# Kernel tuning notes

Measured on AMD Instinct MI355X. Metric: run time of the kernel, lower is better.

## Reference

```python
import jax, jax.numpy as jnp
import numpy as np

N, E = 50000, 250000
SD, VM = 128, 64          # scalar channels, vector multiplicity (irreps: 128x0e + 64x1e)
EA, SH = 64, 4            # edge_attr dim, spherical-harmonics dim (1x0e + 1x1e)
H, FC = 16, 256
HD = FC // H              # head dim = 16
EPS = 1e-5


def _split(x):
    return x[:, :SD], x[:, SD:].reshape(-1, VM, 3)


def _ln(s, V):
    # equivariant layer norm: standardize scalars; RMS-normalize vector norms
    s = (s - s.mean(-1, keepdims=True)) * jax.lax.rsqrt(s.var(-1, keepdims=True) + EPS)
    vn = jax.lax.rsqrt(jnp.mean(jnp.sum(V * V, -1), -1, keepdims=True) + EPS)
    return s, V * vn[..., None]


def setup_inputs() -> dict:
    key = jax.random.key(0)
    ks = iter(jax.random.split(key, 48))
    rn = lambda shp, sc=1.0: jax.random.normal(next(ks), shp, dtype=jnp.float32) * sc
    w = lambda i, o: rn((i, o), 1.0 / np.sqrt(i))
    z = lambda d: jnp.zeros((d,), jnp.float32)
    return dict(
        node_features=rn((N, SD + 3 * VM)),
        edge_attr=rn((E, EA)),
        edge_sh=rn((E, SH)),
        Wq=w(SD, FC), bq=z(FC),
        Wk=w(SD, FC), bk=z(FC),
        We=w(EA, FC), be=z(FC),
        Wv_s=w(SD, SD), bv_s=z(SD), Wv_v=w(VM, VM),
        w_ss=w(SD, SD), w_vv_s=w(VM, SD), w_ssg=w(SD, VM), w_vvg=w(VM, VM),
        b_ms=z(SD), b_mg=z(VM),
        w_sv=w(SD, VM), w_vs=w(VM, VM), w_vvv=w(VM, VM),
        Wo_s=w(SD, SD), bo_s=z(SD), Wo_v=w(VM, VM),
        W1_s=w(SD, SD + VM), b1_s=z(SD + VM), W1_v=w(VM, VM),
        W2_s=w(SD, SD), b2_s=z(SD), W2_v=w(VM, VM),
        edge_index=jax.random.randint(next(ks), (2, E), 0, N, dtype=jnp.int32),
        batch=jnp.zeros((N,), jnp.int32),
    )


def reference(node_features, edge_attr, edge_sh, Wq, bq, Wk, bk, We, be,
              Wv_s, bv_s, Wv_v, w_ss, w_vv_s, w_ssg, w_vvg, b_ms, b_mg,
              w_sv, w_vs, w_vvv, Wo_s, bo_s, Wo_v,
              W1_s, b1_s, W1_v, W2_s, b2_s, W2_v, edge_index, batch):
    src, dst = edge_index[0], edge_index[1]
    ns, nV = _split(node_features)                        # [N,SD], [N,VM,3]

    # per-edge multi-head attention scores (gathered q/k + edge bias term)
    q = (ns[dst] @ Wq + bq).reshape(-1, H, HD)
    k = (ns[src] @ Wk + bk).reshape(-1, H, HD)
    ef = (edge_attr @ We + be).reshape(-1, H, HD)
    scores = ((q * k).sum(-1) + (q * ef).sum(-1)) / np.sqrt(HD)   # [E,H]

    # per-destination-node softmax (replaces the python unique(dst) loop)
    m = jax.ops.segment_max(scores, dst, num_segments=N)
    ex = jnp.exp(scores - m[dst])
    den = jax.ops.segment_sum(ex, dst, num_segments=N)
    attn = (ex / den[dst]).mean(-1, keepdims=True)                # [E,1]

    # v projection (o3.Linear) on source nodes
    vs = ns[src] @ Wv_s + bv_s                                    # [E,SD]
    Vv = jnp.einsum('evk,vu->euk', nV[src], Wv_v)                 # [E,VM,3]

    # message MLP: fully-connected tensor product with edge SH, norm, swish-gate
    shs, shv = edge_sh[:, 0], edge_sh[:, 1:4]
    s_in = vs * shs[:, None]                                      # 0e x 0e -> 0e
    dots = jnp.einsum('evk,ek->ev', Vv, shv)                      # 1e x 1e -> 0e
    ms = s_in @ w_ss + dots @ w_vv_s + b_ms                       # [E,SD] scalars
    mg = s_in @ w_ssg + dots @ w_vvg + b_mg                       # [E,VM] gates
    MV = ((vs @ w_sv)[:, :, None] * shv[:, None, :]               # 0e x 1e -> 1e
          + jnp.einsum('evk,vu->euk', Vv * shs[:, None, None], w_vs)   # 1e x 0e -> 1e
          + jnp.einsum('evk,vu->euk', jnp.cross(Vv, shv[:, None, :]), w_vvv))  # 1e x 1e -> 1e
    sg, MVn = _ln(jnp.concatenate([ms, mg], -1), MV)
    msg_s = jax.nn.silu(sg[:, :SD])
    msg_V = MVn * jax.nn.sigmoid(sg[:, SD:])[:, :, None]

    # attention-weighted scatter-sum aggregation to destination nodes
    agg_s = jax.ops.segment_sum(msg_s * attn, dst, num_segments=N)
    agg_V = jax.ops.segment_sum(msg_V * attn[:, :, None], dst, num_segments=N)

    # out projection + residual + norm1
    x_s = ns + (agg_s @ Wo_s + bo_s)
    x_V = nV + jnp.einsum('nvk,vu->nuk', agg_V, Wo_v)
    x_s, x_V = _ln(x_s, x_V)

    # gated equivariant FFN + residual + norm2
    f = x_s @ W1_s + b1_s                                         # [N,SD+VM]
    fV = jnp.einsum('nvk,vu->nuk', x_V, W1_v)
    gV = fV * jax.nn.sigmoid(f[:, SD:])[:, :, None]
    o_s = x_s + (jax.nn.silu(f[:, :SD]) @ W2_s + b2_s)
    o_V = x_V + jnp.einsum('nvk,vu->nuk', gV, W2_v)
    o_s, o_V = _ln(o_s, o_V)
    return jnp.concatenate([o_s, o_V.reshape(-1, 3 * VM)], -1)
```

## Files before the change

### kernel.cpp

```cpp
#include <hip/hip_runtime.h>
#include <hip/hip_bf16.h>

#define NNODE 50000
#define NEDGE 250000

typedef __hip_bfloat16 bf16;
typedef __attribute__((ext_vector_type(8))) short short8v;
typedef __attribute__((ext_vector_type(4))) float f32x4;

__device__ __forceinline__ float b2f(bf16 x){ return __bfloat162float(x); }
__device__ __forceinline__ bf16  f2b(float x){ return __float2bfloat16(x); }
__device__ __forceinline__ short f2s(float x){ bf16 h=f2b(x); short s; __builtin_memcpy(&s,&h,2); return s; }
__device__ __forceinline__ float s2f(short s){ bf16 h; __builtin_memcpy(&h,&s,2); return b2f(h); }
__device__ __forceinline__ float sigm(float x){ return 1.0f/(1.0f+__expf(-x)); }
__device__ __forceinline__ float wred64(float v){
  #pragma unroll
  for(int o=32;o>0;o>>=1) v+=__shfl_xor(v,o,64);
  return v;
}
__device__ __forceinline__ float gred16(float v){
  v+=__shfl_xor(v,1,64); v+=__shfl_xor(v,2,64); v+=__shfl_xor(v,4,64); v+=__shfl_xor(v,8,64);
  return v;
}
__device__ __forceinline__ int ired64(int v){
  #pragma unroll
  for(int o=32;o>0;o>>=1) v+=__shfl_xor(v,o,64);
  return v;
}
__device__ __forceinline__ int fragOff(int r, int k){
  int kt=k>>5, k32=k&31, half=k32>>4, g=(k32&15)>>2, j=k32&3;
  return (kt<<10)+((r+(g<<4))<<4)+(half<<3)+(j<<1);
}
__device__ __forceinline__ short8v pack8(float4 a, float4 b){
  short8v s; s[0]=f2s(a.x);s[1]=f2s(a.y);s[2]=f2s(a.z);s[3]=f2s(a.w);
  s[4]=f2s(b.x);s[5]=f2s(b.y);s[6]=f2s(b.z);s[7]=f2s(b.w); return s;
}
__device__ __forceinline__ short8v pack8s(short4 a, short4 b){
  short8v s; s[0]=a.x;s[1]=a.y;s[2]=a.z;s[3]=a.w;s[4]=b.x;s[5]=b.y;s[6]=b.z;s[7]=b.w; return s;
}

#define T_WOS 0
#define T_WOV 32
#define T_W1S 40
#define T_W1V 88
#define T_W2S 96
#define T_W2V 128
#define T_WE  136
#define T_WQ  168
#define T_WK  232
#define T_WVS 296
#define T_WSS 328
#define T_WSSG 360
#define T_WSV 376
#define T_WVV 392
#define T_WVVS 400
#define T_WVVG 416
#define T_WVS2 424
#define T_WVVV 432
#define T_TOT 440

__global__ __launch_bounds__(64) void k_prep(
  const float* __restrict__ Wo_s, const float* __restrict__ Wo_v,
  const float* __restrict__ W1_s, const float* __restrict__ W1_v,
  const float* __restrict__ W2_s, const float* __restrict__ W2_v,
  const float* __restrict__ WeM,
  const float* __restrict__ Wq, const float* __restrict__ Wk,
  const float* __restrict__ Wv_s,
  const float* __restrict__ w_ss, const float* __restrict__ w_ssg,
  const float* __restrict__ w_sv,
  const float* __restrict__ Wv_v, const float* __restrict__ w_vv_s,
  const float* __restrict__ w_vvg, const float* __restrict__ w_vs,
  const float* __restrict__ w_vvv,
  short* __restrict__ P)
{
  const int T=blockIdx.x, l=threadIdx.x;
  const float* W; int N, KT, lt;
  if(T<T_WOV){ W=Wo_s; N=128; KT=4; lt=T; }
  else if(T<T_W1S){ W=Wo_v; N=64; KT=2; lt=T-T_WOV; }
  else if(T<T_W1V){ W=W1_s; N=192; KT=4; lt=T-T_W1S; }
  else if(T<T_W2S){ W=W1_v; N=64; KT=2; lt=T-T_W1V; }
  else if(T<T_W2V){ W=W2_s; N=128; KT=4; lt=T-T_W2S; }
  else if(T<T_WE){ W=W2_v; N=64; KT=2; lt=T-T_W2V; }
  else if(T<T_WQ){ W=WeM; N=256; KT=2; lt=T-T_WE; }
  else if(T<T_WK){ W=Wq; N=256; KT=4; lt=T-T_WQ; }
  else if(T<T_WVS){ W=Wk; N=256; KT=4; lt=T-T_WK; }
  else if(T<T_WSS){ W=Wv_s; N=128; KT=4; lt=T-T_WVS; }
  else if(T<T_WSSG){ W=w_ss; N=128; KT=4; lt=T-T_WSS; }
  else if(T<T_WSV){ W=w_ssg; N=64; KT=4; lt=T-T_WSSG; }
  else if(T<T_WVV){ W=w_sv; N=64; KT=4; lt=T-T_WSV; }
  else if(T<T_WVVS){ W=Wv_v; N=64; KT=2; lt=T-T_WVV; }
  else if(T<T_WVVG){ W=w_vv_s; N=128; KT=2; lt=T-T_WVVS; }
  else if(T<T_WVS2){ W=w_vvg; N=64; KT=2; lt=T-T_WVVG; }
  else if(T<T_WVVV){ W=w_vs; N=64; KT=2; lt=T-T_WVS2; }
  else { W=w_vvv; N=64; KT=2; lt=T-T_WVVV; }
  const int nt=lt/KT, kt=lt-nt*KT;
  const int col=nt*16+(l&15);
  short8v o;
  #pragma unroll
  for(int j=0;j<8;j++){
    int k=kt*32+((j>>2)<<4)+((l>>4)<<2)+(j&3);
    o[j]=f2s(W[(size_t)k*N+col]);
  }
  *(short8v*)(P+((size_t)T<<9)+(l<<3))=o;
}

__global__ __launch_bounds__(256) void k1_mfma(
  const float* __restrict__ nf, const short* __restrict__ P,
  const float* __restrict__ bq, const float* __restrict__ bk,
  const float* __restrict__ bvs,
  bf16* __restrict__ Q, bf16* __restrict__ K, short* __restrict__ NREC2)
{
  __shared__ __align__(16) short nsF[4*512];
  __shared__ __align__(16) short vsF[4*512];
  const int t=threadIdx.x, l=t&63, w=t>>6;
  const int n0=blockIdx.x*16;
  for(int i=t;i<512;i+=256){
    int r=i>>5, c=(i&31)<<2;
    const float4 v=*(const float4*)&nf[(size_t)(n0+r)*320+c];
    short4 s; s.x=f2s(v.x); s.y=f2s(v.y); s.z=f2s(v.z); s.w=f2s(v.w);
    *(short4*)((char*)nsF+fragOff(r,c))=s;
  }
  __syncthreads();
  short8v a[4];
  #pragma unroll
  for(int kt=0;kt<4;kt++) a[kt]=*(const short8v*)((const char*)nsF+(kt<<10)+(l<<4));
  #pragma unroll
  for(int ii=0;ii<4;ii++){
    int nt=w+(ii<<2);
    f32x4 accq={0.f,0.f,0.f,0.f}, acck={0.f,0.f,0.f,0.f};
    #pragma unroll
    for(int kt=0;kt<4;kt++){
      short8v bq8=*(const short8v*)(P+(((size_t)(T_WQ+nt*4+kt))<<9)+(l<<3));
      short8v bk8=*(const short8v*)(P+(((size_t)(T_WK+nt*4+kt))<<9)+(l<<3));
      accq=__builtin_amdgcn_mfma_f32_16x16x32_bf16(a[kt],bq8,accq,0,0,0);
      acck=__builtin_amdgcn_mfma_f32_16x16x32_bf16(a[kt],bk8,acck,0,0,0);
    }
    int col=(nt<<4)+(l&15);
    float bqs=bq[col], bks=bk[col];
    #pragma unroll
    for(int r=0;r<4;r++){
      int row=((l>>4)<<2)+r;
      Q[(size_t)(n0+row)*256+col]=f2b(accq[r]+bqs);
      K[(size_t)(n0+row)*256+col]=f2b(acck[r]+bks);
    }
  }
  #pragma unroll
  for(int ii=0;ii<2;ii++){
    int nt=w+(ii<<2);
    f32x4 acc={0.f,0.f,0.f,0.f};
    #pragma unroll
    for(int kt=0;kt<4;kt++){
      short8v b=*(const short8v*)(P+(((size_t)(T_WVS+nt*4+kt))<<9)+(l<<3));
      acc=__builtin_amdgcn_mfma_f32_16x16x32_bf16(a[kt],b,acc,0,0,0);
    }
    int col=(nt<<4)+(l&15);
    float bv=bvs[col];
    #pragma unroll
    for(int r=0;r<4;r++){
      int row=((l>>4)<<2)+r;
      *(short*)((char*)vsF+fragOff(row,col))=f2s(acc[r]+bv);
    }
  }
  __syncthreads();
  #pragma unroll
  for(int kt=0;kt<4;kt++) a[kt]=*(const short8v*)((const char*)vsF+(kt<<10)+(l<<4));
  #pragma unroll
  for(int ii=0;ii<4;ii++){
    int nt=w+(ii<<2);
    int bt;
    if(nt<8) bt=T_WSS+nt*4;
    else if(nt<12) bt=T_WSSG+(nt-8)*4;
    else bt=T_WSV+(nt-12)*4;
    f32x4 acc={0.f,0.f,0.f,0.f};
    #pragma unroll
    for(int kt=0;kt<4;kt++){
      short8v b=*(const short8v*)(P+(((size_t)(bt+kt))<<9)+(l<<3));
      acc=__builtin_amdgcn_mfma_f32_16x16x32_bf16(a[kt],b,acc,0,0,0);
    }
    int col=(nt<<4)+(l&15);
    int lane, sslot;
    if(nt<8){ lane=col&63; sslot=(col>=64)?1:0; }
    else if(nt<12){ lane=col-128; sslot=2; }
    else { lane=col-192; sslot=3; }
    #pragma unroll
    for(int r=0;r<4;r++){
      int row=((l>>4)<<2)+r;
      NREC2[(size_t)(n0+row)*1280 + (lane<<2) + sslot]=f2s(acc[r]);
    }
  }
}

__global__ __launch_bounds__(256) void k2_mfma(
  const float* __restrict__ nf, const short* __restrict__ P,
  short* __restrict__ NREC2)
{
  __shared__ __align__(16) short nvF[6*512];
  __shared__ __align__(16) short vvF[6*512];
  const int t=threadIdx.x, l=t&63, w=t>>6;
  const int n0=blockIdx.x*16;
  for(int i=t;i<3072;i+=256){
    int r=i/192, c=i-r*192;
    int v=c/3, k=c-3*v;
    float x=nf[(size_t)(n0+r)*320+128+c];
    *(short*)((char*)nvF+(k<<11)+fragOff(r,v))=f2s(x);
  }
  __syncthreads();
  #pragma unroll
  for(int jj=0;jj<3;jj++){
    int job=w+(jj<<2);
    int p=job>>2, nt=job&3;
    f32x4 acc={0.f,0.f,0.f,0.f};
    #pragma unroll
    for(int kt=0;kt<2;kt++){
      short8v a2=*(const short8v*)((const char*)nvF+(p<<11)+(kt<<10)+(l<<4));
      short8v b=*(const short8v*)(P+(((size_t)(T_WVV+nt*2+kt))<<9)+(l<<3));
      acc=__builtin_amdgcn_mfma_f32_16x16x32_bf16(a2,b,acc,0,0,0);
    }
    int col=(nt<<4)+(l&15);
    #pragma unroll
    for(int r=0;r<4;r++){
      int row=((l>>4)<<2)+r;
      *(short*)((char*)vvF+(p<<11)+fragOff(row,col))=f2s(acc[r]);
    }
  }
  __syncthreads();
  #pragma unroll
  for(int jj=0;jj<15;jj++){
    int job=w+(jj<<2);
    int p=job/20, r20=job-p*20;
    int nt, bt, G0;
    if(r20<8){ nt=r20; bt=T_WVVS+nt*2; G0=0; }
    else if(r20<12){ nt=r20-8; bt=T_WVVG+nt*2; G0=1; }
    else if(r20<16){ nt=r20-12; bt=T_WVS2+nt*2; G0=2; }
    else { nt=r20-16; bt=T_WVVV+nt*2; G0=3; }
    f32x4 acc={0.f,0.f,0.f,0.f};
    #pragma unroll
    for(int kt=0;kt<2;kt++){
      short8v a2=*(const short8v*)((const char*)vvF+(p<<11)+(kt<<10)+(l<<4));
      short8v b=*(const short8v*)(P+(((size_t)(bt+kt))<<9)+(l<<3));
      acc=__builtin_amdgcn_mfma_f32_16x16x32_bf16(a2,b,acc,0,0,0);
    }
    int col=(nt<<4)+(l&15);
    int G;
    if(G0==0)      G = p*2 + (col>=64 ? 1 : 0);
    else if(G0==1) G = 6 + p;
    else if(G0==2) G = 9 + p;
    else           G = 12 + p;
    int lane = col & 63;
    int addr = ((1+(G>>2))<<8) + (lane<<2) + (G&3);
    #pragma unroll
    for(int r=0;r<4;r++){
      int row=((l>>4)<<2)+r;
      NREC2[(size_t)(n0+row)*1280 + addr]=f2s(acc[r]);
    }
  }
}

__global__ __launch_bounds__(256) void k_hist(const int* __restrict__ eidx, int* __restrict__ counts){
  int e=blockIdx.x*256+threadIdx.x;
  if(e<NEDGE) atomicAdd(&counts[eidx[NEDGE+e]],1);
}

#define SCAN_NB 196

__global__ __launch_bounds__(256) void k_scan1(const int* __restrict__ counts, int* __restrict__ bsum){
  const int t=threadIdx.x, ln=t&63, wid=t>>6;
  int idx=blockIdx.x*256+t;
  int v=(idx<NNODE)?counts[idx]:0;
  int s=ired64(v);
  __shared__ int ws[4];
  if(ln==0) ws[wid]=s;
  __syncthreads();
  if(t==0) bsum[blockIdx.x]=ws[0]+ws[1]+ws[2]+ws[3];
}

__global__ __launch_bounds__(256) void k_scan2(const int* __restrict__ bsum, int* __restrict__ boff){
  const int t=threadIdx.x, ln=t&63, wid=t>>6;
  int v=(t<SCAN_NB)?bsum[t]:0;
  int incl=v;
  #pragma unroll
  for(int o=1;o<64;o<<=1){ int x=__shfl_up(incl,o,64); if(ln>=o) incl+=x; }
  __shared__ int wtot[4], wpre[4];
  if(ln==63) wtot[wid]=incl;
  __syncthreads();
  if(t==0){ int s=0; for(int k=0;k<4;k++){ wpre[k]=s; s+=wtot[k]; } }
  __syncthreads();
  if(t<SCAN_NB) boff[t]=wpre[wid]+incl-v;
}

__global__ __launch_bounds__(256) void k_scan3(const int* __restrict__ counts, const int* __restrict__ boff,
                                               int* __restrict__ off, int* __restrict__ cursor){
  const int t=threadIdx.x, ln=t&63, wid=t>>6;
  int idx=blockIdx.x*256+t;
  int v=(idx<NNODE)?counts[idx]:0;
  int incl=v;
  #pragma unroll
  for(int o=1;o<64;o<<=1){ int x=__shfl_up(incl,o,64); if(ln>=o) incl+=x; }
  __shared__ int wtot[4], wpre[4];
  if(ln==63) wtot[wid]=incl;
  __syncthreads();
  if(t==0){ int s=0; for(int k=0;k<4;k++){ wpre[k]=s; s+=wtot[k]; } }
  __syncthreads();
  int excl=boff[blockIdx.x]+wpre[wid]+incl-v;
  if(idx<NNODE){ off[idx]=excl; cursor[idx]=excl; }
  if(blockIdx.x==SCAN_NB-1 && t==255) off[NNODE]=NEDGE;
}

__global__ __launch_bounds__(256) void k_scatter(
  const int* __restrict__ eidx, const float* __restrict__ esh,
  int* __restrict__ cursor, int* __restrict__ eord,
  int* __restrict__ srcs, int* __restrict__ dsts, float* __restrict__ eshs)
{
  int e=blockIdx.x*256+threadIdx.x;
  if(e<NEDGE){
    int d=eidx[NEDGE+e];
    int pos=atomicAdd(&cursor[d],1);
    eord[pos]=e;
    srcs[pos]=eidx[e];
    dsts[pos]=d;
    *(float4*)&eshs[(size_t)pos*4]=*(const float4*)&esh[(size_t)e*4];
  }
}

__global__ __launch_bounds__(256) void k3_mfma(
  const float* __restrict__ eattr,
  const int* __restrict__ EORD, const int* __restrict__ SRCs, const int* __restrict__ DSTs,
  const short* __restrict__ P, const float* __restrict__ be,
  const bf16* __restrict__ Q, const bf16* __restrict__ K,
  float* __restrict__ SC)
{
  __shared__ __align__(16) short aeF[2*512];
  __shared__ __align__(16) float ef[16][260];
  __shared__ int sed[16], ssrc[16], sdst[16];
  const int t=threadIdx.x, l=t&63, w=t>>6;
  const int e0=blockIdx.x*16;
  if(t<16){
    sed[t]=EORD[e0+t];
    ssrc[t]=SRCs[e0+t];
    sdst[t]=DSTs[e0+t];
  }
  __syncthreads();
  {
    int r=t>>4, c4=(t&15)<<2;
    const float4 v=*(const float4*)&eattr[(size_t)sed[r]*64+c4];
    short4 s; s.x=f2s(v.x); s.y=f2s(v.y); s.z=f2s(v.z); s.w=f2s(v.w);
    *(short4*)((char*)aeF+fragOff(r,c4))=s;
  }
  __syncthreads();
  {
    short8v a0=*(const short8v*)((const char*)aeF+(l<<4));
    short8v a1=*(const short8v*)((const char*)aeF+1024+(l<<4));
    #pragma unroll
    for(int ii=0;ii<4;ii++){
      int nt=w+(ii<<2);
      f32x4 acc={0.f,0.f,0.f,0.f};
      short8v b0=*(const short8v*)(P+(((size_t)(T_WE+nt*2+0))<<9)+(l<<3));
      short8v b1=*(const short8v*)(P+(((size_t)(T_WE+nt*2+1))<<9)+(l<<3));
      acc=__builtin_amdgcn_mfma_f32_16x16x32_bf16(a0,b0,acc,0,0,0);
      acc=__builtin_amdgcn_mfma_f32_16x16x32_bf16(a1,b1,acc,0,0,0);
      int col=(nt<<4)+(l&15);
      float bv=be[col];
      #pragma unroll
      for(int r=0;r<4;r++){ int row=((l>>4)<<2)+r; ef[row][col]=acc[r]+bv; }
    }
  }
  __syncthreads();
  {
    const int h=l&15, qt=l>>4;
    const int ch=h*16+(qt<<2);
    #pragma unroll
    for(int j=0;j<4;j++){
      int el=w*4+j;
      int s=ssrc[el], d=sdst[el];
      short4 qs=*(const short4*)((const short*)Q+(size_t)d*256+ch);
      short4 ks=*(const short4*)((const short*)K+(size_t)s*256+ch);
      const float4 e4=*(const float4*)&ef[el][ch];
      float p = s2f(qs.x)*(s2f(ks.x)+e4.x)
              + s2f(qs.y)*(s2f(ks.y)+e4.y)
              + s2f(qs.z)*(s2f(ks.z)+e4.z)
              + s2f(qs.w)*(s2f(ks.w)+e4.w);
      p += __shfl_xor(p,16,64);
      p += __shfl_xor(p,32,64);
      if(qt==0) SC[(size_t)(e0+el)*16+h]=p*0.25f;
    }
  }
}

__global__ __launch_bounds__(256) void k5_att(
  const float* __restrict__ SC, const int* __restrict__ OFF,
  float* __restrict__ ATTs)
{
  const int l=threadIdx.x&63;
  const int n=blockIdx.x*4+(threadIdx.x>>6);
  const int beg=OFF[n], end=OFF[n+1];
  const int j=l>>4, h=l&15;
  float mh=-1e30f;
  for(int i=beg+j;i<end;i+=4) mh=fmaxf(mh, SC[(size_t)i*16+h]);
  mh=fmaxf(mh,__shfl_xor(mh,16,64));
  mh=fmaxf(mh,__shfl_xor(mh,32,64));
  float dh=0.f;
  for(int i=beg+j;i<end;i+=4) dh+=__expf(SC[(size_t)i*16+h]-mh);
  dh+=__shfl_xor(dh,16,64);
  dh+=__shfl_xor(dh,32,64);
  float rdh=(end>beg)?1.f/dh:0.f;
  for(int i0=beg;i0<end;i0+=4){
    int i=i0+j;
    float a=0.f; bool act=(i<end);
    if(act) a=__expf(SC[(size_t)i*16+h]-mh)*rdh;
    a=gred16(a);
    if(h==0 && act) ATTs[i]=a*(1.f/16.f);
  }
}

__global__ __launch_bounds__(256) void k6_agg(
  const int* __restrict__ SRCs, const float* __restrict__ ESHs,
  const short* __restrict__ NREC2, const float* __restrict__ ATTs,
  const int* __restrict__ OFF,
  const float* __restrict__ b_ms, const float* __restrict__ b_mg,
  float* __restrict__ AGS, float* __restrict__ AGV)
{
  const int l = threadIdx.x & 63;
  const int n = blockIdx.x*4 + (threadIdx.x>>6);
  const int beg=OFF[n], end=OFF[n+1];
  const float bmsa=b_ms[l], bmsb=b_ms[64+l], bmgv=b_mg[l];

  float as0=0.f,as1=0.f,av0acc=0.f,av1acc=0.f,av2acc=0.f;
  for(int i=beg;i<end;i++){
    const int s=SRCs[i];
    const float att=ATTs[i];
    const float4 sh4=*(const float4*)&ESHs[(size_t)i*4];
    const float shs=sh4.x, sh0=sh4.y, sh1=sh4.z, sh2=sh4.w;

    const short* R = NREC2 + (size_t)s*1280 + (l<<2);
    const short4 q0=*(const short4*)(R);
    const short4 q1=*(const short4*)(R+256);
    const short4 q2=*(const short4*)(R+512);
    const short4 q3=*(const short4*)(R+768);
    const short4 q4=*(const short4*)(R+1024);

    float msa = shs*s2f(q0.x) + s2f(q1.x)*sh0 + s2f(q1.z)*sh1 + s2f(q2.x)*sh2 + bmsa;
    float msb = shs*s2f(q0.y) + s2f(q1.y)*sh0 + s2f(q1.w)*sh1 + s2f(q2.y)*sh2 + bmsb;
    float mgv = shs*s2f(q0.z) + s2f(q2.z)*sh0 + s2f(q2.w)*sh1 + s2f(q3.x)*sh2 + bmgv;

    float sum = wred64(msa+msb+mgv);
    float sq  = wred64(msa*msa+msb*msb+mgv*mgv);
    float mean = sum*(1.f/192.f);
    float var  = sq*(1.f/192.f) - mean*mean;
    float rs   = rsqrtf(var + 1e-5f);

    const float svv=s2f(q0.w);
    const float w0=s2f(q3.y), w1=s2f(q3.z), w2=s2f(q3.w);
    const float c0=s2f(q4.x), c1=s2f(q4.y), c2=s2f(q4.z);
    float cr0 = c1*sh2 - c2*sh1;
    float cr1 = c2*sh0 - c0*sh2;
    float cr2 = c0*sh1 - c1*sh0;
    float mv0 = svv*sh0 + shs*w0 + cr0;
    float mv1 = svv*sh1 + shs*w1 + cr1;
    float mv2 = svv*sh2 + shs*w2 + cr2;
    float vsq = wred64(mv0*mv0+mv1*mv1+mv2*mv2);
    float vn  = rsqrtf(vsq*(1.f/64.f) + 1e-5f);

    float sga=(msa-mean)*rs, sgb=(msb-mean)*rs, sgg=(mgv-mean)*rs;
    float wV = vn * sigm(sgg) * att;
    as0 += sga*sigm(sga)*att;
    as1 += sgb*sigm(sgb)*att;
    av0acc += mv0*wV;
    av1acc += mv1*wV;
    av2acc += mv2*wV;
  }
  AGS[(size_t)n*128+l]     =as0;
  AGS[(size_t)n*128+64+l]  =as1;
  AGV[(size_t)n*192+l]     =av0acc;
  AGV[(size_t)n*192+64+l]  =av1acc;
  AGV[(size_t)n*192+128+l] =av2acc;
}

__global__ __launch_bounds__(256) void k7_mfma(
  const float* __restrict__ nf,
  const float* __restrict__ AGS, const float* __restrict__ AGV,
  const short* __restrict__ P,
  const float* __restrict__ bo_s, const float* __restrict__ b1_s, const float* __restrict__ b2_s,
  float* __restrict__ out)
{
  __shared__ float xs[16][132];
  __shared__ short xvh[16][200];
  __shared__ short ffh[16][204];
  __shared__ __align__(16) short asA[4*512];
  __shared__ __align__(16) short avA[6*512];
  __shared__ float smean[16], srs[16], svn[16];
  const int t=threadIdx.x, l=t&63, w=t>>6;
  const int n0=blockIdx.x*16;
  const int lam=t&63, kt4=t>>6;
  const int fr=lam&15, fg=lam>>4;

  for(int i=t;i<2048;i+=256){ int r=i>>7,c=i&127; xs[r][c]=nf[(size_t)(n0+r)*320+c]; }
  for(int i=t;i<3072;i+=256){ int r=i/192,cc=i-r*192; int k=cc>>6,u=cc&63; xvh[r][cc]=f2s(nf[(size_t)(n0+r)*320+128+u*3+k]); }
  {
    const float* base=&AGS[(size_t)(n0+fr)*128 + (kt4<<5) + (fg<<2)];
    float4 va=*(const float4*)base, vb=*(const float4*)(base+16);
    *(short8v*)((char*)asA+(kt4<<10)+(lam<<4))=pack8(va,vb);
  }
  for(int i=t;i<384;i+=256){
    int seg=i>>6, lm=i&63, r=lm&15, g=lm>>4;
    int p=seg>>1, k2=seg&1;
    const float* base=&AGV[(size_t)(n0+r)*192 + (p<<6) + (k2<<5) + (g<<2)];
    float4 va=*(const float4*)base, vb=*(const float4*)(base+16);
    *(short8v*)((char*)avA+(seg<<10)+(lm<<4))=pack8(va,vb);
  }
  __syncthreads();

  {
    short8v a[4];
    #pragma unroll
    for(int kt=0;kt<4;kt++) a[kt]=*(const short8v*)((const char*)asA+(kt<<10)+(l<<4));
    #pragma unroll
    for(int ii=0;ii<2;ii++){
      int nt=w+(ii<<2);
      f32x4 acc={0.f,0.f,0.f,0.f};
      #pragma unroll
      for(int kt=0;kt<4;kt++){
        short8v b=*(const short8v*)(P+(((size_t)(T_WOS+nt*4+kt))<<9)+(l<<3));
        acc=__builtin_amdgcn_mfma_f32_16x16x32_bf16(a[kt],b,acc,0,0,0);
      }
      int col=(nt<<4)+(l&15);
      float bv=bo_s[col];
      #pragma unroll
      for(int r=0;r<4;r++){ int row=((l>>4)<<2)+r; xs[row][col]+=acc[r]+bv; }
    }
    #pragma unroll
    for(int ii=0;ii<3;ii++){
      int tid=w*3+ii, p=tid>>2, nt2=tid&3;
      f32x4 acc={0.f,0.f,0.f,0.f};
      #pragma unroll
      for(int kt=0;kt<2;kt++){
        short8v a2=*(const short8v*)((const char*)avA+(((p<<1)+kt)<<10)+(l<<4));
        short8v b=*(const short8v*)(P+(((size_t)(T_WOV+nt2*2+kt))<<9)+(l<<3));
        acc=__builtin_amdgcn_mfma_f32_16x16x32_bf16(a2,b,acc,0,0,0);
      }
      int col=(p<<6)+(nt2<<4)+(l&15);
      #pragma unroll
      for(int r=0;r<4;r++){
        int row=((l>>4)<<2)+r;
        float x=s2f(xvh[row][col]);
        xvh[row][col]=f2s(x+acc[r]);
      }
    }
  }
  __syncthreads();

  {
    const int nn=t>>4, g=t&15;
    float sum=0,sq=0;
    #pragma unroll
    for(int j=0;j<8;j++){ float x=xs[nn][g+16*j]; sum+=x; sq+=x*x; }
    sum=gred16(sum); sq=gred16(sq);
    float mean=sum*(1.f/128.f);
    float var=sq*(1.f/128.f)-mean*mean;
    float vsq=0;
    #pragma unroll
    for(int j=0;j<12;j++){ float x=s2f(xvh[nn][g+16*j]); vsq+=x*x; }
    vsq=gred16(vsq);
    if(g==0){ smean[nn]=mean; srs[nn]=rsqrtf(var+1e-5f); svn[nn]=rsqrtf(vsq*(1.f/64.f)+1e-5f); }
  }
  __syncthreads();

  for(int i=t;i<512;i+=256){
    int r=i>>5, c=(i&31)<<2;
    float m=smean[r], rs=srs[r];
    float4 v=*(float4*)&xs[r][c];
    v.x=(v.x-m)*rs; v.y=(v.y-m)*rs; v.z=(v.z-m)*rs; v.w=(v.w-m)*rs;
    *(float4*)&xs[r][c]=v;
  }
  for(int i=t;i<768;i+=256){
    int r=i/48, c=(i-r*48)<<2;
    float vn=svn[r];
    short4 sv4=*(short4*)&xvh[r][c];
    sv4.x=f2s(s2f(sv4.x)*vn); sv4.y=f2s(s2f(sv4.y)*vn);
    sv4.z=f2s(s2f(sv4.z)*vn); sv4.w=f2s(s2f(sv4.w)*vn);
    *(short4*)&xvh[r][c]=sv4;
  }
  __syncthreads();
  {
    float4 va=*(const float4*)&xs[fr][(kt4<<5)+(fg<<2)];
    float4 vb=*(const float4*)&xs[fr][(kt4<<5)+16+(fg<<2)];
    *(short8v*)((char*)asA+(kt4<<10)+(lam<<4))=pack8(va,vb);
  }
  for(int i=t;i<384;i+=256){
    int seg=i>>6, lm=i&63, r=lm&15, g=lm>>4;
    int p=seg>>1, k2=seg&1;
    short4 sa=*(const short4*)&xvh[r][(p<<6)+(k2<<5)+(g<<2)];
    short4 sb=*(const short4*)&xvh[r][(p<<6)+(k2<<5)+16+(g<<2)];
    *(short8v*)((char*)avA+(seg<<10)+(lm<<4))=pack8s(sa,sb);
  }
  __syncthreads();

  {
    short8v a[4];
    #pragma unroll
    for(int kt=0;kt<4;kt++) a[kt]=*(const short8v*)((const char*)asA+(kt<<10)+(l<<4));
    #pragma unroll
    for(int ii=0;ii<3;ii++){
      int nt=w+(ii<<2);
      f32x4 acc={0.f,0.f,0.f,0.f};
      #pragma unroll
      for(int kt=0;kt<4;kt++){
        short8v b=*(const short8v*)(P+(((size_t)(T_W1S+nt*4+kt))<<9)+(l<<3));
        acc=__builtin_amdgcn_mfma_f32_16x16x32_bf16(a[kt],b,acc,0,0,0);
      }
      int col=(nt<<4)+(l&15);
      float bv=b1_s[col];
      #pragma unroll
      for(int r=0;r<4;r++){ int row=((l>>4)<<2)+r; ffh[row][col]=f2s(acc[r]+bv); }
    }
  }
  __syncthreads();

  f32x4 g4acc[3];
  {
    #pragma unroll
    for(int ii=0;ii<3;ii++){
      int tid=w*3+ii, p=tid>>2, nt2=tid&3;
      f32x4 acc={0.f,0.f,0.f,0.f};
      #pragma unroll
      for(int kt=0;kt<2;kt++){
        short8v a2=*(const short8v*)((const char*)avA+(((p<<1)+kt)<<10)+(l<<4));
        short8v b=*(const short8v*)(P+(((size_t)(T_W1V+nt2*2+kt))<<9)+(l<<3));
        acc=__builtin_amdgcn_mfma_f32_16x16x32_bf16(a2,b,acc,0,0,0);
      }
      g4acc[ii]=acc;
    }
    for(int i=t;i<512;i+=256){
      int r=i>>5, c=(i&31)<<2;
      short4 sv4=*(short4*)&ffh[r][c];
      float x0=s2f(sv4.x), x1=s2f(sv4.y), x2=s2f(sv4.z), x3=s2f(sv4.w);
      sv4.x=f2s(x0*sigm(x0)); sv4.y=f2s(x1*sigm(x1)); sv4.z=f2s(x2*sigm(x2)); sv4.w=f2s(x3*sigm(x3));
      *(short4*)&ffh[r][c]=sv4;
    }
  }
  __syncthreads();

  {
    short4 sa=*(const short4*)&ffh[fr][(kt4<<5)+(fg<<2)];
    short4 sb=*(const short4*)&ffh[fr][(kt4<<5)+16+(fg<<2)];
    *(short8v*)((char*)asA+(kt4<<10)+(lam<<4))=pack8s(sa,sb);
  }
  {
    #pragma unroll
    for(int ii=0;ii<3;ii++){
      int tid=w*3+ii, nt2=tid&3;
      int uu=(nt2<<4)+(l&15);
      #pragma unroll
      for(int r=0;r<4;r++){
        int row=((l>>4)<<2)+r;
        g4acc[ii][r]*=sigm(s2f(ffh[row][128+uu]));
      }
    }
  }
  __syncthreads();

  {
    #pragma unroll
    for(int ii=0;ii<3;ii++){
      int tid=w*3+ii, p=tid>>2, nt2=tid&3;
      int uu=(nt2<<4)+(l&15);
      #pragma unroll
      for(int r=0;r<4;r++){
        int row=((l>>4)<<2)+r;
        ffh[row][(p<<6)+uu]=f2s(g4acc[ii][r]);
      }
    }
  }
  __syncthreads();
  for(int i=t;i<384;i+=256){
    int seg=i>>6, lm=i&63, r=lm&15, g=lm>>4;
    int p=seg>>1, k2=seg&1;
    short4 sa=*(const short4*)&ffh[r][(p<<6)+(k2<<5)+(g<<2)];
    short4 sb=*(const short4*)&ffh[r][(p<<6)+(k2<<5)+16+(g<<2)];
    *(short8v*)((char*)avA+(seg<<10)+(lm<<4))=pack8s(sa,sb);
  }
  __syncthreads();

  {
    short8v a[4];
    #pragma unroll
    for(int kt=0;kt<4;kt++) a[kt]=*(const short8v*)((const char*)asA+(kt<<10)+(l<<4));
    #pragma unroll
    for(int ii=0;ii<2;ii++){
      int nt=w+(ii<<2);
      f32x4 acc={0.f,0.f,0.f,0.f};
      #pragma unroll
      for(int kt=0;kt<4;kt++){
        short8v b=*(const short8v*)(P+(((size_t)(T_W2S+nt*4+kt))<<9)+(l<<3));
        acc=__builtin_amdgcn_mfma_f32_16x16x32_bf16(a[kt],b,acc,0,0,0);
      }
      int col=(nt<<4)+(l&15);
      float bv=b2_s[col];
      #pragma unroll
      for(int r=0;r<4;r++){ int row=((l>>4)<<2)+r; xs[row][col]+=acc[r]+bv; }
    }
    #pragma unroll
    for(int ii=0;ii<3;ii++){
      int tid=w*3+ii, p=tid>>2, nt2=tid&3;
      f32x4 acc={0.f,0.f,0.f,0.f};
      #pragma unroll
      for(int kt=0;kt<2;kt++){
        short8v a2=*(const short8v*)((const char*)avA+(((p<<1)+kt)<<10)+(l<<4));
        short8v b=*(const short8v*)(P+(((size_t)(T_W2V+nt2*2+kt))<<9)+(l<<3));
        acc=__builtin_amdgcn_mfma_f32_16x16x32_bf16(a2,b,acc,0,0,0);
      }
      int col=(p<<6)+(nt2<<4)+(l&15);
      #pragma unroll
      for(int r=0;r<4;r++){
        int row=((l>>4)<<2)+r;
        float x=s2f(xvh[row][col]);
        xvh[row][col]=f2s(x+acc[r]);
      }
    }
  }
  __syncthreads();

  {
    const int nn=t>>4, g=t&15;
    float sum=0,sq=0;
    #pragma unroll
    for(int j=0;j<8;j++){ float x=xs[nn][g+16*j]; sum+=x; sq+=x*x; }
    sum=gred16(sum); sq=gred16(sq);
    float mean=sum*(1.f/128.f);
    float var=sq*(1.f/128.f)-mean*mean;
    float vsq=0;
    #pragma unroll
    for(int j=0;j<12;j++){ float x=s2f(xvh[nn][g+16*j]); vsq+=x*x; }
    vsq=gred16(vsq);
    if(g==0){ smean[nn]=mean; srs[nn]=rsqrtf(var+1e-5f); svn[nn]=rsqrtf(vsq*(1.f/64.f)+1e-5f); }
  }
  __syncthreads();

  for(int i=t;i<16*320;i+=256){
    int nn=i/320, c=i-nn*320;
    float v;
    if(c<128) v=(xs[nn][c]-smean[nn])*srs[nn];
    else { int j=c-128; int u=j/3, k=j-u*3; v=s2f(xvh[nn][(k<<6)+u])*svn[nn]; }
    out[(size_t)(n0+nn)*320+c]=v;
  }
}

extern "C" void kernel_launch(void* const* d_in, const int* in_sizes, int n_in,
                              void* d_out, int out_size, void* d_ws, size_t ws_size,
                              hipStream_t stream)
{
  (void)in_sizes; (void)n_in; (void)out_size; (void)ws_size;
  const float* nf    =(const float*)d_in[0];
  const float* eattr =(const float*)d_in[1];
  const float* esh   =(const float*)d_in[2];
  const float* Wq    =(const float*)d_in[3];  const float* bq  =(const float*)d_in[4];
  const float* Wk    =(const float*)d_in[5];  const float* bk  =(const float*)d_in[6];
  const float* We    =(const float*)d_in[7];  const float* be  =(const float*)d_in[8];
  const float* Wv_s  =(const float*)d_in[9];  const float* bv_s=(const float*)d_in[10];
  const float* Wv_v  =(const float*)d_in[11];
  const float* w_ss  =(const float*)d_in[12]; const float* w_vv_s=(const float*)d_in[13];
  const float* w_ssg =(const float*)d_in[14]; const float* w_vvg =(const float*)d_in[15];
  const float* b_ms  =(const float*)d_in[16]; const float* b_mg  =(const float*)d_in[17];
  const float* w_sv  =(const float*)d_in[18]; const float* w_vs  =(const float*)d_in[19];
  const float* w_vvv =(const float*)d_in[20];
  const float* Wo_s  =(const float*)d_in[21]; const float* bo_s  =(const float*)d_in[22];
  const float* Wo_v  =(const float*)d_in[23];
  const float* W1_s  =(const float*)d_in[24]; const float* b1_s  =(const float*)d_in[25];
  const float* W1_v  =(const float*)d_in[26];
  const float* W2_s  =(const float*)d_in[27]; const float* b2_s  =(const float*)d_in[28];
  const float* W2_v  =(const float*)d_in[29];
  const int*   eidx  =(const int*)d_in[30];
  float* out=(float*)d_out;

  char* w=(char*)d_ws;
  bf16* Q    =(bf16*)w;  w+=(size_t)NNODE*256*2;
  bf16* Kb   =(bf16*)w;  w+=(size_t)NNODE*256*2;
  short* NREC2=(short*)w; w+=(size_t)NNODE*1280*2;
  float* SC  =(float*)w; w+=(size_t)NEDGE*16*4;
  float* ESHs=(float*)w; w+=(size_t)NEDGE*4*4;
  float* ATTs=(float*)w; w+=(size_t)NEDGE*4;
  float* AGS =(float*)w; w+=(size_t)NNODE*128*4;
  float* AGV =(float*)w; w+=(size_t)NNODE*192*4;
  short* P   =(short*)w; w+=(size_t)T_TOT*512*2;
  int* COUNTS=(int*)w;   w+=(size_t)NNODE*4;
  int* OFFb  =(int*)w;   w+=(size_t)(NNODE+1)*4;
  int* CURSOR=(int*)w;   w+=(size_t)NNODE*4;
  int* EORDb =(int*)w;   w+=(size_t)NEDGE*4;
  int* SRCs  =(int*)w;   w+=(size_t)NEDGE*4;
  int* BSUM  =(int*)w;   w+=(size_t)256*4;
  int* BOFF  =(int*)w;   w+=(size_t)256*4;
  int* DSTs = (int*)ATTs;

  hipMemsetAsync(COUNTS,0,(size_t)NNODE*4,stream);

  k_prep    <<<T_TOT,64,0,stream>>>(Wo_s,Wo_v,W1_s,W1_v,W2_s,W2_v,We,
                                    Wq,Wk,Wv_s,w_ss,w_ssg,w_sv,
                                    Wv_v,w_vv_s,w_vvg,w_vs,w_vvv,P);
  k_hist    <<<(NEDGE+255)/256,256,0,stream>>>(eidx,COUNTS);
  k_scan1   <<<SCAN_NB,256,0,stream>>>(COUNTS,BSUM);
  k_scan2   <<<1,256,0,stream>>>(BSUM,BOFF);
  k_scan3   <<<SCAN_NB,256,0,stream>>>(COUNTS,BOFF,OFFb,CURSOR);
  k_scatter <<<(NEDGE+255)/256,256,0,stream>>>(eidx,esh,CURSOR,EORDb,SRCs,DSTs,ESHs);
  k1_mfma   <<<NNODE/16,256,0,stream>>>(nf,P,bq,bk,bv_s,Q,Kb,NREC2);
  k2_mfma   <<<NNODE/16,256,0,stream>>>(nf,P,NREC2);
  k3_mfma   <<<NEDGE/16,256,0,stream>>>(eattr,EORDb,SRCs,DSTs,P,be,Q,Kb,SC);
  k5_att    <<<NNODE/4,256,0,stream>>>(SC,OFFb,ATTs);
  k6_agg    <<<NNODE/4,256,0,stream>>>(SRCs,ESHs,NREC2,ATTs,OFFb,b_ms,b_mg,AGS,AGV);
  k7_mfma   <<<NNODE/16,256,0,stream>>>(nf,AGS,AGV,P,bo_s,b1_s,b2_s,out);
}
```

Before: 467.2 us.

## Store aggregates as bf16 and process 32 nodes per 512-thread k7 block

The aggregation kernel now writes its per-node scalar and vector sums as bf16 instead of fp32, halving the intermediate buffer traffic between k6 and k7. k7 was already converting these to bf16 for MFMA, so the precision loss is mostly the same. k7 is also reorganised into 512-thread blocks covering two 16-row tiles (32 nodes), with bounds guards for the tail block. This doubles shared-memory use per block, which may lower occupancy.

```diff
diff --git a/kernel.cpp b/kernel.cpp
--- a/kernel.cpp
+++ b/kernel.cpp
@@ -417,7 +417,7 @@
   const short* __restrict__ NREC2, const float* __restrict__ ATTs,
   const int* __restrict__ OFF,
   const float* __restrict__ b_ms, const float* __restrict__ b_mg,
-  float* __restrict__ AGS, float* __restrict__ AGV)
+  short* __restrict__ AGSh, short* __restrict__ AGVh)
 {
   const int l = threadIdx.x & 63;
   const int n = blockIdx.x*4 + (threadIdx.x>>6);
@@ -468,54 +468,65 @@
     av1acc += mv1*wV;
     av2acc += mv2*wV;
   }
-  AGS[(size_t)n*128+l]     =as0;
-  AGS[(size_t)n*128+64+l]  =as1;
-  AGV[(size_t)n*192+l]     =av0acc;
-  AGV[(size_t)n*192+64+l]  =av1acc;
-  AGV[(size_t)n*192+128+l] =av2acc;
-}
-
-__global__ __launch_bounds__(256) void k7_mfma(
+  AGSh[(size_t)n*128+l]     =f2s(as0);
+  AGSh[(size_t)n*128+64+l]  =f2s(as1);
+  AGVh[(size_t)n*192+l]     =f2s(av0acc);
+  AGVh[(size_t)n*192+64+l]  =f2s(av1acc);
+  AGVh[(size_t)n*192+128+l] =f2s(av2acc);
+}
+
+#define K7NBLK ((NNODE+31)/32)
+__global__ __launch_bounds__(512) void k7_mfma(
   const float* __restrict__ nf,
-  const float* __restrict__ AGS, const float* __restrict__ AGV,
+  const short* __restrict__ AGSh, const short* __restrict__ AGVh,
   const short* __restrict__ P,
   const float* __restrict__ bo_s, const float* __restrict__ b1_s, const float* __restrict__ b2_s,
   float* __restrict__ out)
 {
-  __shared__ float xs[16][132];
-  __shared__ short xvh[16][200];
-  __shared__ short ffh[16][204];
-  __shared__ __align__(16) short asA[4*512];
-  __shared__ __align__(16) short avA[6*512];
-  __shared__ float smean[16], srs[16], svn[16];
+  __shared__ float xs[32][132];
+  __shared__ short xvh[32][200];
+  __shared__ short ffh[32][204];
+  __shared__ __align__(16) short asA[2][4*512];
+  __shared__ __align__(16) short avA[2][6*512];
+  __shared__ float smean[32], srs[32], svn[32];
   const int t=threadIdx.x, l=t&63, w=t>>6;
-  const int n0=blockIdx.x*16;
-  const int lam=t&63, kt4=t>>6;
-  const int fr=lam&15, fg=lam>>4;
-
-  for(int i=t;i<2048;i+=256){ int r=i>>7,c=i&127; xs[r][c]=nf[(size_t)(n0+r)*320+c]; }
-  for(int i=t;i<3072;i+=256){ int r=i/192,cc=i-r*192; int k=cc>>6,u=cc&63; xvh[r][cc]=f2s(nf[(size_t)(n0+r)*320+128+u*3+k]); }
-  {
-    const float* base=&AGS[(size_t)(n0+fr)*128 + (kt4<<5) + (fg<<2)];
-    float4 va=*(const float4*)base, vb=*(const float4*)(base+16);
-    *(short8v*)((char*)asA+(kt4<<10)+(lam<<4))=pack8(va,vb);
-  }
-  for(int i=t;i<384;i+=256){
-    int seg=i>>6, lm=i&63, r=lm&15, g=lm>>4;
-    int p=seg>>1, k2=seg&1;
-    const float* base=&AGV[(size_t)(n0+r)*192 + (p<<6) + (k2<<5) + (g<<2)];
-    float4 va=*(const float4*)base, vb=*(const float4*)(base+16);
-    *(short8v*)((char*)avA+(seg<<10)+(lm<<4))=pack8(va,vb);
+  const int rt=w>>2, wq=w&3;
+  const int n0=blockIdx.x*32;
+  const int seg=t>>6, lam=t&63;
+  const int sfr=lam&15, sfg=lam>>4;
+
+  for(int i=t;i<4096;i+=512){ int r=i>>7,c=i&127; int nd=n0+r; xs[r][c]=(nd<NNODE)?nf[(size_t)nd*320+c]:0.f; }
+  for(int i=t;i<6144;i+=512){ int r=i/192,cc=i-r*192; int k=cc>>6,u=cc&63; int nd=n0+r; xvh[r][cc]=(nd<NNODE)?f2s(nf[(size_t)nd*320+128+u*3+k]):(short)0; }
+  {
+    int srt=seg>>2, skt=seg&3;
+    int nd=n0+srt*16+sfr;
+    short4 va={0,0,0,0}, vb={0,0,0,0};
+    if(nd<NNODE){
+      const short* b=AGSh+(size_t)nd*128+skt*32+(sfg<<2);
+      va=*(const short4*)b; vb=*(const short4*)(b+16);
+    }
+    *(short8v*)((char*)asA[srt]+(skt<<10)+(lam<<4))=pack8s(va,vb);
+  }
+  for(int i=t;i<768;i+=512){
+    int srt=i/384, s6=(i-srt*384)>>6, lm=i&63, r=lm&15, g=lm>>4;
+    int p=s6>>1, k2=s6&1;
+    int nd=n0+srt*16+r;
+    short4 va={0,0,0,0}, vb={0,0,0,0};
+    if(nd<NNODE){
+      const short* b=AGVh+(size_t)nd*192+(p<<6)+(k2<<5)+(g<<2);
+      va=*(const short4*)b; vb=*(const short4*)(b+16);
+    }
+    *(short8v*)((char*)avA[srt]+(s6<<10)+(lm<<4))=pack8s(va,vb);
   }
   __syncthreads();
 
   {
     short8v a[4];
     #pragma unroll
-    for(int kt=0;kt<4;kt++) a[kt]=*(const short8v*)((const char*)asA+(kt<<10)+(l<<4));
+    for(int kt=0;kt<4;kt++) a[kt]=*(const short8v*)((const char*)asA[rt]+(kt<<10)+(l<<4));
     #pragma unroll
     for(int ii=0;ii<2;ii++){
-      int nt=w+(ii<<2);
+      int nt=wq+(ii<<2);
       f32x4 acc={0.f,0.f,0.f,0.f};
       #pragma unroll
       for(int kt=0;kt<4;kt++){
@@ -525,22 +536,22 @@
       int col=(nt<<4)+(l&15);
       float bv=bo_s[col];
       #pragma unroll
-      for(int r=0;r<4;r++){ int row=((l>>4)<<2)+r; xs[row][col]+=acc[r]+bv; }
+      for(int r=0;r<4;r++){ int row=rt*16+((l>>4)<<2)+r; xs[row][col]+=acc[r]+bv; }
     }
     #pragma unroll
     for(int ii=0;ii<3;ii++){
-      int tid=w*3+ii, p=tid>>2, nt2=tid&3;
+      int tid=wq*3+ii, p=tid>>2, nt2=tid&3;
       f32x4 acc={0.f,0.f,0.f,0.f};
       #pragma unroll
       for(int kt=0;kt<2;kt++){
-        short8v a2=*(const short8v*)((const char*)avA+(((p<<1)+kt)<<10)+(l<<4));
+        short8v a2=*(const short8v*)((const char*)avA[rt]+(((p<<1)+kt)<<10)+(l<<4));
         short8v b=*(const short8v*)(P+(((size_t)(T_WOV+nt2*2+kt))<<9)+(l<<3));
         acc=__builtin_amdgcn_mfma_f32_16x16x32_bf16(a2,b,acc,0,0,0);
       }
       int col=(p<<6)+(nt2<<4)+(l&15);
       #pragma unroll
       for(int r=0;r<4;r++){
-        int row=((l>>4)<<2)+r;
+        int row=rt*16+((l>>4)<<2)+r;
         float x=s2f(xvh[row][col]);
         xvh[row][col]=f2s(x+acc[r]);
       }
@@ -564,14 +575,14 @@
   }
   __syncthreads();
 
-  for(int i=t;i<512;i+=256){
+  for(int i=t;i<1024;i+=512){
     int r=i>>5, c=(i&31)<<2;
     float m=smean[r], rs=srs[r];
     float4 v=*(float4*)&xs[r][c];
     v.x=(v.x-m)*rs; v.y=(v.y-m)*rs; v.z=(v.z-m)*rs; v.w=(v.w-m)*rs;
     *(float4*)&xs[r][c]=v;
   }
-  for(int i=t;i<768;i+=256){
+  for(int i=t;i<1536;i+=512){
     int r=i/48, c=(i-r*48)<<2;
     float vn=svn[r];
     short4 sv4=*(short4*)&xvh[r][c];
@@ -581,26 +592,27 @@
   }
   __syncthreads();
   {
-    float4 va=*(const float4*)&xs[fr][(kt4<<5)+(fg<<2)];
-    float4 vb=*(const float4*)&xs[fr][(kt4<<5)+16+(fg<<2)];
-    *(short8v*)((char*)asA+(kt4<<10)+(lam<<4))=pack8(va,vb);
-  }
-  for(int i=t;i<384;i+=256){
-    int seg=i>>6, lm=i&63, r=lm&15, g=lm>>4;
-    int p=seg>>1, k2=seg&1;
-    short4 sa=*(const short4*)&xvh[r][(p<<6)+(k2<<5)+(g<<2)];
-    short4 sb=*(const short4*)&xvh[r][(p<<6)+(k2<<5)+16+(g<<2)];
-    *(short8v*)((char*)avA+(seg<<10)+(lm<<4))=pack8s(sa,sb);
+    int srt=seg>>2, skt=seg&3;
+    float4 va=*(const float4*)&xs[srt*16+sfr][(skt<<5)+(sfg<<2)];
+    float4 vb=*(const float4*)&xs[srt*16+sfr][(skt<<5)+16+(sfg<<2)];
+    *(short8v*)((char*)asA[srt]+(skt<<10)+(lam<<4))=pack8(va,vb);
+  }
+  for(int i=t;i<768;i+=512){
+    int srt=i/384, s6=(i-srt*384)>>6, lm=i&63, r=lm&15, g=lm>>4;
+    int p=s6>>1, k2=s6&1;
+    short4 sa=*(const short4*)&xvh[srt*16+r][(p<<6)+(k2<<5)+(g<<2)];
+    short4 sb=*(const short4*)&xvh[srt*16+r][(p<<6)+(k2<<5)+16+(g<<2)];
+    *(short8v*)((char*)avA[srt]+(s6<<10)+(lm<<4))=pack8s(sa,sb);
   }
   __syncthreads();
 
   {
     short8v a[4];
     #pragma unroll
-    for(int kt=0;kt<4;kt++) a[kt]=*(const short8v*)((const char*)asA+(kt<<10)+(l<<4));
+    for(int kt=0;kt<4;kt++) a[kt]=*(const short8v*)((const char*)asA[rt]+(kt<<10)+(l<<4));
     #pragma unroll
     for(int ii=0;ii<3;ii++){
-      int nt=w+(ii<<2);
+      int nt=wq+(ii<<2);
       f32x4 acc={0.f,0.f,0.f,0.f};
       #pragma unroll
       for(int kt=0;kt<4;kt++){
@@ -610,7 +622,7 @@
       int col=(nt<<4)+(l&15);
       float bv=b1_s[col];
       #pragma unroll
-      for(int r=0;r<4;r++){ int row=((l>>4)<<2)+r; ffh[row][col]=f2s(acc[r]+bv); }
+      for(int r=0;r<4;r++){ int row=rt*16+((l>>4)<<2)+r; ffh[row][col]=f2s(acc[r]+bv); }
     }
   }
   __syncthreads();
@@ -619,17 +631,17 @@
   {
     #pragma unroll
     for(int ii=0;ii<3;ii++){
-      int tid=w*3+ii, p=tid>>2, nt2=tid&3;
+      int tid=wq*3+ii, p=tid>>2, nt2=tid&3;
       f32x4 acc={0.f,0.f,0.f,0.f};
       #pragma unroll
       for(int kt=0;kt<2;kt++){
-        short8v a2=*(const short8v*)((const char*)avA+(((p<<1)+kt)<<10)+(l<<4));
+        short8v a2=*(const short8v*)((const char*)avA[rt]+(((p<<1)+kt)<<10)+(l<<4));
         short8v b=*(const short8v*)(P+(((size_t)(T_W1V+nt2*2+kt))<<9)+(l<<3));
         acc=__builtin_amdgcn_mfma_f32_16x16x32_bf16(a2,b,acc,0,0,0);
       }
       g4acc[ii]=acc;
     }
-    for(int i=t;i<512;i+=256){
+    for(int i=t;i<1024;i+=512){
       int r=i>>5, c=(i&31)<<2;
       short4 sv4=*(short4*)&ffh[r][c];
       float x0=s2f(sv4.x), x1=s2f(sv4.y), x2=s2f(sv4.z), x3=s2f(sv4.w);
@@ -640,18 +652,19 @@
   __syncthreads();
 
   {
-    short4 sa=*(const short4*)&ffh[fr][(kt4<<5)+(fg<<2)];
-    short4 sb=*(const short4*)&ffh[fr][(kt4<<5)+16+(fg<<2)];
-    *(short8v*)((char*)asA+(kt4<<10)+(lam<<4))=pack8s(sa,sb);
+    int srt=seg>>2, skt=seg&3;
+    short4 sa=*(const short4*)&ffh[srt*16+sfr][(skt<<5)+(sfg<<2)];
+    short4 sb=*(const short4*)&ffh[srt*16+sfr][(skt<<5)+16+(sfg<<2)];
+    *(short8v*)((char*)asA[srt]+(skt<<10)+(lam<<4))=pack8s(sa,sb);
   }
   {
     #pragma unroll
     for(int ii=0;ii<3;ii++){
-      int tid=w*3+ii, nt2=tid&3;
+      int tid=wq*3+ii, nt2=tid&3;
       int uu=(nt2<<4)+(l&15);
       #pragma unroll
       for(int r=0;r<4;r++){
-        int row=((l>>4)<<2)+r;
+        int row=rt*16+((l>>4)<<2)+r;
         g4acc[ii][r]*=sigm(s2f(ffh[row][128+uu]));
       }
     }
@@ -661,32 +674,32 @@
   {
     #pragma unroll
     for(int ii=0;ii<3;ii++){
-      int tid=w*3+ii, p=tid>>2, nt2=tid&3;
+      int tid=wq*3+ii, p=tid>>2, nt2=tid&3;
       int uu=(nt2<<4)+(l&15);
       #pragma unroll
       for(int r=0;r<4;r++){
-        int row=((l>>4)<<2)+r;
+        int row=rt*16+((l>>4)<<2)+r;
         ffh[row][(p<<6)+uu]=f2s(g4acc[ii][r]);
       }
     }
   }
   __syncthreads();
-  for(int i=t;i<384;i+=256){
-    int seg=i>>6, lm=i&63, r=lm&15, g=lm>>4;
-    int p=seg>>1, k2=seg&1;
-    short4 sa=*(const short4*)&ffh[r][(p<<6)+(k2<<5)+(g<<2)];
-    short4 sb=*(const short4*)&ffh[r][(p<<6)+(k2<<5)+16+(g<<2)];
-    *(short8v*)((char*)avA+(seg<<10)+(lm<<4))=pack8s(sa,sb);
+  for(int i=t;i<768;i+=512){
+    int srt=i/384, s6=(i-srt*384)>>6, lm=i&63, r=lm&15, g=lm>>4;
+    int p=s6>>1, k2=s6&1;
+    short4 sa=*(const short4*)&ffh[srt*16+r][(p<<6)+(k2<<5)+(g<<2)];
+    short4 sb=*(const short4*)&ffh[srt*16+r][(p<<6)+(k2<<5)+16+(g<<2)];
+    *(short8v*)((char*)avA[srt]+(s6<<10)+(lm<<4))=pack8s(sa,sb);
   }
   __syncthreads();
 
   {
     short8v a[4];
     #pragma unroll
-    for(int kt=0;kt<4;kt++) a[kt]=*(const short8v*)((const char*)asA+(kt<<10)+(l<<4));
+    for(int kt=0;kt<4;kt++) a[kt]=*(const short8v*)((const char*)asA[rt]+(kt<<10)+(l<<4));
     #pragma unroll
     for(int ii=0;ii<2;ii++){
-      int nt=w+(ii<<2);
+      int nt=wq+(ii<<2);
       f32x4 acc={0.f,0.f,0.f,0.f};
       #pragma unroll
       for(int kt=0;kt<4;kt++){
@@ -696,22 +709,22 @@
       int col=(nt<<4)+(l&15);
       float bv=b2_s[col];
       #pragma unroll
-      for(int r=0;r<4;r++){ int row=((l>>4)<<2)+r; xs[row][col]+=acc[r]+bv; }
+      for(int r=0;r<4;r++){ int row=rt*16+((l>>4)<<2)+r; xs[row][col]+=acc[r]+bv; }
     }
     #pragma unroll
     for(int ii=0;ii<3;ii++){
-      int tid=w*3+ii, p=tid>>2, nt2=tid&3;
+      int tid=wq*3+ii, p=tid>>2, nt2=tid&3;
       f32x4 acc={0.f,0.f,0.f,0.f};
       #pragma unroll
       for(int kt=0;kt<2;kt++){
-        short8v a2=*(const short8v*)((const char*)avA+(((p<<1)+kt)<<10)+(l<<4));
+        short8v a2=*(const short8v*)((const char*)avA[rt]+(((p<<1)+kt)<<10)+(l<<4));
         short8v b=*(const short8v*)(P+(((size_t)(T_W2V+nt2*2+kt))<<9)+(l<<3));
         acc=__builtin_amdgcn_mfma_f32_16x16x32_bf16(a2,b,acc,0,0,0);
       }
       int col=(p<<6)+(nt2<<4)+(l&15);
       #pragma unroll
       for(int r=0;r<4;r++){
-        int row=((l>>4)<<2)+r;
+        int row=rt*16+((l>>4)<<2)+r;
         float x=s2f(xvh[row][col]);
         xvh[row][col]=f2s(x+acc[r]);
       }
@@ -735,12 +748,15 @@
   }
   __syncthreads();
 
-  for(int i=t;i<16*320;i+=256){
+  for(int i=t;i<10240;i+=512){
     int nn=i/320, c=i-nn*320;
-    float v;
-    if(c<128) v=(xs[nn][c]-smean[nn])*srs[nn];
-    else { int j=c-128; int u=j/3, k=j-u*3; v=s2f(xvh[nn][(k<<6)+u])*svn[nn]; }
-    out[(size_t)(n0+nn)*320+c]=v;
+    int nd=n0+nn;
+    if(nd<NNODE){
+      float v;
+      if(c<128) v=(xs[nn][c]-smean[nn])*srs[nn];
+      else { int j=c-128; int u=j/3, k=j-u*3; v=s2f(xvh[nn][(k<<6)+u])*svn[nn]; }
+      out[(size_t)nd*320+c]=v;
+    }
   }
 }
 
@@ -778,8 +794,8 @@
   float* SC  =(float*)w; w+=(size_t)NEDGE*16*4;
   float* ESHs=(float*)w; w+=(size_t)NEDGE*4*4;
   float* ATTs=(float*)w; w+=(size_t)NEDGE*4;
-  float* AGS =(float*)w; w+=(size_t)NNODE*128*4;
-  float* AGV =(float*)w; w+=(size_t)NNODE*192*4;
+  short* AGSh=(short*)w; w+=(size_t)NNODE*128*2;
+  short* AGVh=(short*)w; w+=(size_t)NNODE*192*2;
   short* P   =(short*)w; w+=(size_t)T_TOT*512*2;
   int* COUNTS=(int*)w;   w+=(size_t)NNODE*4;
   int* OFFb  =(int*)w;   w+=(size_t)(NNODE+1)*4;
@@ -804,6 +820,6 @@
   k2_mfma   <<<NNODE/16,256,0,stream>>>(nf,P,NREC2);
   k3_mfma   <<<NEDGE/16,256,0,stream>>>(eattr,EORDb,SRCs,DSTs,P,be,Q,Kb,SC);
   k5_att    <<<NNODE/4,256,0,stream>>>(SC,OFFb,ATTs);
-  k6_agg    <<<NNODE/4,256,0,stream>>>(SRCs,ESHs,NREC2,ATTs,OFFb,b_ms,b_mg,AGS,AGV);
-  k7_mfma   <<<NNODE/16,256,0,stream>>>(nf,AGS,AGV,P,bo_s,b1_s,b2_s,out);
-}
+  k6_agg    <<<NNODE/4,256,0,stream>>>(SRCs,ESHs,NREC2,ATTs,OFFb,b_ms,b_mg,AGSh,AGVh);
+  k7_mfma   <<<K7NBLK,512,0,stream>>>(nf,AGSh,AGVh,P,bo_s,b1_s,b2_s,out);
+}
```

After: 469.5 us. About the same (+0.5%).
